# Kernel optimization log

Measured on AMD Instinct MI355X. Metric: run time of the kernel, lower is better.

## Reference

```python
import jax, jax.numpy as jnp
import numpy as np

N, E, F_NODE, F_EDGE = 100000, 400000, 64, 16
HID, HEADS, L, G, FP = 128, 4, 4, 1024, 2048
DH = HID // HEADS
T, K = 5, 32
EPS = 1e-5
NEG_SLOPE = 0.2


def _gat(x, src, dst, ea, Wl, bl, Wr, br, We, att, bias):
    """GATv2Conv (PyG semantics, eval mode): x_l=lin_l(x_src), x_r=lin_r(x_dst),
    e = att . leaky_relu(x_l[src] + x_r[dst] + lin_edge(edge_attr)),
    alpha = segment-softmax over dst, out = scatter-sum(alpha * x_l[src]) + bias."""
    n = x.shape[0]
    xl = (x @ Wl + bl).reshape(n, HEADS, DH)
    xr = (x @ Wr + br).reshape(n, HEADS, DH)
    ee = (ea @ We).reshape(-1, HEADS, DH)
    e = jax.nn.leaky_relu(xl[src] + xr[dst] + ee, NEG_SLOPE)  # [E,H,D]
    score = jnp.einsum('ehd,hd->eh', e, att)                   # [E,H]
    m = jax.ops.segment_max(score, dst, num_segments=n)        # stable softmax
    p = jnp.exp(score - m[dst])
    denom = jax.ops.segment_sum(p, dst, num_segments=n)
    alpha = p / (denom[dst] + 1e-16)
    out = jax.ops.segment_sum(alpha[:, :, None] * xl[src], dst, num_segments=n)
    return out.reshape(n, HID) + bias


def _bn_elu(h, g, b):
    # BatchNorm over the node dimension (training-mode batch stats) + ELU
    mu = h.mean(0)
    var = h.var(0)
    return jax.nn.elu((h - mu) / jnp.sqrt(var + EPS) * g + b)


def setup_inputs() -> dict:
    key = jax.random.key(0)
    ks = jax.random.split(key, 16)
    s_in = 1.0 / np.sqrt(F_NODE)
    s_h = 1.0 / np.sqrt(HID)
    s_e = 1.0 / np.sqrt(F_EDGE)
    Lh = L - 1
    return dict(
        x=jax.random.normal(ks[0], (N, F_NODE), jnp.float32),
        edge_index=jax.random.randint(ks[1], (2, E), 0, N),
        edge_attr=jax.random.normal(ks[2], (E, F_EDGE), jnp.float32),
        batch=jnp.sort(jax.random.randint(ks[3], (N,), 0, G)),
        morgan_fp=(jax.random.uniform(ks[4], (G, FP)) < 0.1).astype(jnp.float32),
        fp_idx=jnp.arange(T * K).reshape(T, K),
        Wl0=jax.random.normal(ks[5], (F_NODE, HID)) * s_in,
        bl0=jnp.zeros((HID,)),
        Wr0=jax.random.normal(ks[6], (F_NODE, HID)) * s_in,
        br0=jnp.zeros((HID,)),
        We0=jax.random.normal(ks[7], (F_EDGE, HID)) * s_e,
        att0=jax.random.normal(ks[8], (HEADS, DH)) * s_h,
        bias0=jnp.zeros((HID,)),
        g0=jnp.ones((HID,)),
        b0=jnp.zeros((HID,)),
        Wl=jax.random.normal(ks[9], (Lh, HID, HID)) * s_h,
        bl=jnp.zeros((Lh, HID)),
        Wr=jax.random.normal(ks[10], (Lh, HID, HID)) * s_h,
        br=jnp.zeros((Lh, HID)),
        We=jax.random.normal(ks[11], (Lh, F_EDGE, HID)) * s_e,
        att=jax.random.normal(ks[12], (Lh, HEADS, DH)) * s_h,
        biasc=jnp.zeros((Lh, HID)),
        g=jnp.ones((Lh, HID)),
        b=jnp.zeros((Lh, HID)),
        tw1=jax.random.normal(ks[13], (T, HID + K, HID)) / np.sqrt(HID + K),
        tb1=jnp.zeros((T, HID)),
        tw2=jax.random.normal(ks[14], (T, HID, 1)) * s_h,
        tb2=jnp.zeros((T, 1)),
    )


def reference(x, edge_index, edge_attr, batch, morgan_fp, fp_idx,
              Wl0, bl0, Wr0, br0, We0, att0, bias0, g0, b0,
              Wl, bl, Wr, br, We, att, biasc, g, b,
              tw1, tb1, tw2, tb2):
    src, dst = edge_index[0], edge_index[1]
    h = _bn_elu(_gat(x, src, dst, edge_attr, Wl0, bl0, Wr0, br0, We0, att0, bias0), g0, b0)
    for i in range(L - 1):  # residual stacked GATv2 layers
        h = _bn_elu(_gat(h, src, dst, edge_attr, Wl[i], bl[i], Wr[i], br[i],
                         We[i], att[i], biasc[i]), g[i], b[i]) + h
    counts = jax.ops.segment_sum(jnp.ones((h.shape[0],), h.dtype), batch, num_segments=G)
    emb = jax.ops.segment_sum(h, batch, num_segments=G) / jnp.maximum(counts, 1.0)[:, None]
    outs = []
    for t in range(T):  # per-task heads on [graph_emb ; selected fp bits]
        fused = jnp.concatenate([emb, morgan_fp[:, fp_idx[t]]], axis=1)
        hm = jax.nn.relu(fused @ tw1[t] + tb1[t])
        outs.append(hm @ tw2[t] + tb2[t])
    return jnp.concatenate(outs, axis=1)  # [G, T]
```

## Files before the change

### kernel.cpp

```cpp
#include <hip/hip_runtime.h>
#include <hip/hip_bf16.h>

#define N_NODES 100000
#define N_EDGES 400000
#define F_NODE_ 64
#define F_EDGE_ 16
#define HID_ 128
#define N_GRAPH 1024
#define N_TASK 5
#define NSTRIPE 32

typedef unsigned short u16;
typedef __attribute__((ext_vector_type(8))) short frag8;
typedef __attribute__((ext_vector_type(4))) float f32x4;
typedef __attribute__((ext_vector_type(2))) float f32x2;

__device__ __forceinline__ float bu2f(u16 v){ return __uint_as_float(((unsigned)v) << 16); }
__device__ __forceinline__ float2 bp2f(unsigned u){
  return make_float2(__uint_as_float(u << 16), __uint_as_float(u & 0xFFFF0000u));
}
__device__ __forceinline__ f32x2 bp2v(unsigned u){
  f32x2 r; r.x = __uint_as_float(u << 16); r.y = __uint_as_float(u & 0xFFFF0000u); return r;
}
__device__ __forceinline__ u16 f2bu(float f){
  __hip_bfloat16 h = __float2bfloat16(f);
  return *(u16*)&h;
}
__device__ __forceinline__ unsigned packbf(float a, float b){
  return (unsigned)f2bu(a) | ((unsigned)f2bu(b) << 16);
}
__device__ __forceinline__ f32x2 pmax2(f32x2 a, f32x2 b){
#if defined(__has_builtin)
#if __has_builtin(__builtin_elementwise_max)
  return __builtin_elementwise_max(a, b);
#else
  f32x2 r; r.x = fmaxf(a.x,b.x); r.y = fmaxf(a.y,b.y); return r;
#endif
#else
  f32x2 r; r.x = fmaxf(a.x,b.x); r.y = fmaxf(a.y,b.y); return r;
#endif
}

struct WZ12 { const float* src[12]; u16* dst[12]; int Ks[12]; int Kd[12]; };

#define CAST_BLKS ((N_NODES*F_NODE_ + 255)/256)
#define EG256 ((N_EDGES + 255)/256)
#define GOFF_BLKS ((N_GRAPH + 1 + 255)/256)
#define WSWZ_BLKS (12*64)
__global__ __launch_bounds__(256) void k_cast_hist(const float* __restrict__ s, u16* __restrict__ d,
                                                   const int* __restrict__ ei, int* __restrict__ counts,
                                                   const int* __restrict__ batch, int* __restrict__ goff,
                                                   WZ12 p){
  int b = blockIdx.x;
  if (b < CAST_BLKS){
    int i = b*256 + threadIdx.x;
    if (i < N_NODES*F_NODE_) d[i] = f2bu(s[i]);
  } else if (b < CAST_BLKS + EG256){
    int e = (b - CAST_BLKS)*256 + threadIdx.x;
    if (e < N_EDGES) atomicAdd(&counts[ei[N_EDGES + e]], 1);
  } else if (b < CAST_BLKS + EG256 + GOFF_BLKS){
    int g = (b - CAST_BLKS - EG256)*256 + threadIdx.x;
    if (g <= N_GRAPH){
      int lo = 0, hi = N_NODES;
      while (lo < hi){
        int mid = (lo + hi) >> 1;
        if (batch[mid] < g) lo = mid + 1; else hi = mid;
      }
      goff[g] = lo;
    }
  } else {
    int bb = b - CAST_BLKS - EG256 - GOFF_BLKS;
    const int sW = bb >> 6;
    const int Kd = p.Kd[sW], Ks = p.Ks[sW];
    int i = (bb & 63)*256 + threadIdx.x;
    if (i >= Kd*128) return;
    int k = i >> 7, n = i & 127;
    float v = (k < Ks) ? p.src[sW][k*128 + n] : 0.f;
    int kk = k & 31, c = k >> 5;
    int quad = kk >> 3, j = kk & 7;
    int nt = n >> 4;
    int lane = quad*16 + (n & 15);
    p.dst[sW][(((c*8 + nt)*64) + lane)*8 + j] = f2bu(v);
  }
}

#define GEMM_GRID ((N_NODES + 127)/128)
#define EPROJ_GRID ((N_EDGES + 127)/128)
__global__ __launch_bounds__(256) void k_gemm_eproj(const u16* __restrict__ A,
                                                    const u16* __restrict__ Wzl,
                                                    const u16* __restrict__ Wzr,
                                                    const float* __restrict__ bl,
                                                    const float* __restrict__ br,
                                                    u16* __restrict__ Cl,
                                                    u16* Cr,
                                                    int M, int K,
                                                    const u16* __restrict__ ea16,
                                                    const u16* __restrict__ Wez,
                                                    u16* __restrict__ eproj){
  __shared__ u16 WS[128*128];
  const int t = threadIdx.x;
  const int b = blockIdx.x;
  if (b < 2*GEMM_GRID){
    const int which = (b >= GEMM_GRID);
    const int bx = which ? b - GEMM_GRID : b;
    const u16*   Wz   = which ? Wzr : Wzl;
    const float* bias = which ? br  : bl;
    u16*         C    = which ? Cr  : Cl;
    {
      const uint4* src = (const uint4*)Wz;
      uint4* dst = (uint4*)WS;
      const int n = (K*128) >> 3;
      for (int i = t; i < n; i += 256) dst[i] = src[i];
    }
    __syncthreads();
    const int w = t >> 6, l = t & 63;
    const int m = l & 15, quad = l >> 4;
    const int rowA0 = bx*128 + w*32 + m;
    const int rowA1 = rowA0 + 16;
    f32x4 acc[2][8];
    #pragma unroll
    for (int i=0;i<2;i++)
      #pragma unroll
      for (int j=0;j<8;j++) acc[i][j] = (f32x4){0.f,0.f,0.f,0.f};
    const int KC = K >> 5;
    for (int c = 0; c < KC; c++){
      frag8 a0 = {}, a1 = {};
      if (rowA0 < M) a0 = *(const frag8*)(A + (size_t)rowA0*K + c*32 + quad*8);
      if (rowA1 < M) a1 = *(const frag8*)(A + (size_t)rowA1*K + c*32 + quad*8);
      #pragma unroll
      for (int nt = 0; nt < 8; nt++){
        frag8 bfr = *(const frag8*)&WS[(((c*8 + nt)*64) + l)*8];
        acc[0][nt] = __builtin_amdgcn_mfma_f32_16x16x32_bf16(a0, bfr, acc[0][nt], 0,0,0);
        acc[1][nt] = __builtin_amdgcn_mfma_f32_16x16x32_bf16(a1, bfr, acc[1][nt], 0,0,0);
      }
    }
    float bcv[8];
    #pragma unroll
    for (int nt=0; nt<8; nt++) bcv[nt] = bias[nt*16 + m];
    __syncthreads();
    const int sXor = quad << 4;
    #pragma unroll
    for (int rt = 0; rt < 2; rt++){
      #pragma unroll
      for (int r = 0; r < 4; r++){
        const int row = w*32 + rt*16 + quad*4 + r;
        #pragma unroll
        for (int nt = 0; nt < 8; nt++){
          const int col = nt*16 + m;
          WS[row*128 + (col ^ sXor)] = f2bu(acc[rt][nt][r] + bcv[nt]);
        }
      }
    }
    __syncthreads();
    #pragma unroll
    for (int i = 0; i < 8; i++){
      const int idx = i*256 + t;
      const int row = idx >> 4, k16 = idx & 15;
      const int grp = (k16*8) ^ (((row>>2)&3)<<4);
      const int grow = bx*128 + row;
      if (grow < M)
        *(uint4*)(C + (size_t)grow*128 + k16*8) = *(const uint4*)&WS[row*128 + grp];
    }
  } else {
    const int bx = b - 2*GEMM_GRID;
    {
      const uint4* s4 = (const uint4*)Wez;
      uint4* d4 = (uint4*)WS;
      for (int i = t; i < 512; i += 256) d4[i] = s4[i];
    }
    __syncthreads();
    const int w = t >> 6, l = t & 63, m = l & 15, quad = l >> 4;
    const int row0 = bx*128 + w*32 + m;
    const int row1 = row0 + 16;
    f32x4 acc[2][8];
    #pragma unroll
    for (int i=0;i<2;i++)
      #pragma unroll
      for (int j=0;j<8;j++) acc[i][j] = (f32x4){0.f,0.f,0.f,0.f};
    frag8 a0 = {}, a1 = {};
    if (quad < 2){
      a0 = *(const frag8*)(ea16 + (size_t)row0*16 + quad*8);
      a1 = *(const frag8*)(ea16 + (size_t)row1*16 + quad*8);
    }
    #pragma unroll
    for (int nt = 0; nt < 8; nt++){
      frag8 bfr = *(const frag8*)&WS[(nt*64 + l)*8];
      acc[0][nt] = __builtin_amdgcn_mfma_f32_16x16x32_bf16(a0, bfr, acc[0][nt], 0,0,0);
      acc[1][nt] = __builtin_amdgcn_mfma_f32_16x16x32_bf16(a1, bfr, acc[1][nt], 0,0,0);
    }
    __syncthreads();
    const int sXor = quad << 4;
    #pragma unroll
    for (int rt = 0; rt < 2; rt++){
      #pragma unroll
      for (int r = 0; r < 4; r++){
        const int row = w*32 + rt*16 + quad*4 + r;
        #pragma unroll
        for (int nt = 0; nt < 8; nt++){
          const int col = nt*16 + m;
          WS[row*128 + (col ^ sXor)] = f2bu(acc[rt][nt][r]);
        }
      }
    }
    __syncthreads();
    #pragma unroll
    for (int i = 0; i < 8; i++){
      const int idx = i*256 + t;
      const int row = idx >> 4, k16 = idx & 15;
      const int grp = (k16*8) ^ (((row>>2)&3)<<4);
      *(uint4*)(eproj + ((size_t)(bx*128 + row))*128 + k16*8) = *(const uint4*)&WS[row*128 + grp];
    }
  }
}

__global__ __launch_bounds__(512) void k_scan1(const int* __restrict__ counts,
                                               int* __restrict__ incl,
                                               int* __restrict__ bsum){
  __shared__ int s[512];
  const int t = threadIdx.x;
  int i = blockIdx.x*512 + t;
  int v = (i < N_NODES) ? counts[i] : 0;
  s[t] = v;
  __syncthreads();
  for (int off = 1; off < 512; off <<= 1){
    int x = (t >= off) ? s[t - off] : 0;
    __syncthreads();
    s[t] += x;
    __syncthreads();
  }
  if (i < N_NODES) incl[i] = s[t];
  if (t == 511) bsum[blockIdx.x] = s[511];
}

__global__ __launch_bounds__(512) void k_scan3(const int* __restrict__ counts,
                                               const int* __restrict__ incl,
                                               const int* __restrict__ bsum, int nb,
                                               int* __restrict__ offsets,
                                               int* __restrict__ cursor){
  __shared__ int sb[256];
  const int t = threadIdx.x;
  if (t < 256) sb[t] = (t < nb) ? bsum[t] : 0;
  __syncthreads();
  for (int off = 1; off < 256; off <<= 1){
    int x = 0;
    if (t < 256 && t >= off) x = sb[t - off];
    __syncthreads();
    if (t < 256) sb[t] += x;
    __syncthreads();
  }
  int i = blockIdx.x*512 + t;
  if (i >= N_NODES) return;
  int pre = (blockIdx.x == 0) ? 0 : sb[blockIdx.x - 1];
  int o = pre + incl[i];
  offsets[i + 1] = o;
  cursor[i]      = o - counts[i];
  if (i == 0) offsets[0] = 0;
}

__global__ __launch_bounds__(256) void k_scatter(const int* __restrict__ ei,
                                                 int* __restrict__ cursor,
                                                 int* __restrict__ ssrc,
                                                 const float* __restrict__ ea,
                                                 u16* __restrict__ ea16){
  int e = blockIdx.x*256 + threadIdx.x;
  if (e >= N_EDGES) return;
  int dst = ei[N_EDGES + e];
  int pos = atomicAdd(&cursor[dst], 1);
  ssrc[pos] = ei[e];
  const float* s = ea + (size_t)e*F_EDGE_;
  unsigned p[8];
  #pragma unroll
  for (int k=0;k<8;k++) p[k] = packbf(s[2*k], s[2*k+1]);
  uint4* d4 = (uint4*)(ea16 + (size_t)pos*16);
  d4[0] = make_uint4(p[0],p[1],p[2],p[3]);
  d4[1] = make_uint4(p[4],p[5],p[6],p[7]);
}

#define GAT_GRID (N_NODES/8)
__global__ __launch_bounds__(128) void k_gat_ep(const u16* __restrict__ xl,
                                                unsigned* xr_aggr,
                                                const u16* __restrict__ eproj,
                                                const float* __restrict__ att,
                                                const int* __restrict__ offsets,
                                                const int* __restrict__ ssrc,
                                                float* __restrict__ stats){
  __shared__ float red[4][264];
  const int t = threadIdx.x;
  const int wave = t >> 6, lane = t & 63;
  const int half = lane >> 5, l32 = lane & 31;
  const int c0 = l32*4;
  const float4 av = *(const float4*)(att + c0);
  const f32x2 avlo = {av.x, av.y}, avhi = {av.z, av.w};
  float ss0=0.f, ss1=0.f, ss2=0.f, ss3=0.f;
  float qq0=0.f, qq1=0.f, qq2=0.f, qq3=0.f;

  for (int k = 0; k < 2; k++){
    const int node = blockIdx.x*8 + wave*4 + k*2 + half;
    const uint2 xru = *(const uint2*)(xr_aggr + (size_t)node*64 + l32*2);
    const f32x2 xr0 = bp2v(xru.x), xr1 = bp2v(xru.y);
    f32x2 acc0 = {0.f,0.f}, acc1 = {0.f,0.f};
    float den = 0.f;
    const int beg = offsets[node], end = offsets[node+1];
    int it = (end - beg + 3) >> 2;
    int oit = __shfl_xor(it, 32);
    const int maxit = it > oit ? it : oit;
    int i = beg;
    for (int n = 0; n < maxit; n++, i += 4){
      const int mm = end - i;
      int ib = (mm > 0) ? i : beg;
      ib = ib < N_EDGES ? ib : N_EDGES - 1;
      const int i0 = ib;
      const int i1 = (mm > 1) ? i+1 : ib;
      const int i2 = (mm > 2) ? i+2 : ib;
      const int i3 = (mm > 3) ? i+3 : ib;
      const int s0 = ssrc[i0], s1 = ssrc[i1], s2 = ssrc[i2], s3 = ssrc[i3];
      const uint2 e0 = *(const uint2*)(eproj + (size_t)i0*128 + c0);
      const uint2 e1 = *(const uint2*)(eproj + (size_t)i1*128 + c0);
      const uint2 e2 = *(const uint2*)(eproj + (size_t)i2*128 + c0);
      const uint2 e3 = *(const uint2*)(eproj + (size_t)i3*128 + c0);
      const uint2 x0 = *(const uint2*)(xl + (size_t)s0*HID_ + c0);
      const uint2 x1 = *(const uint2*)(xl + (size_t)s1*HID_ + c0);
      const uint2 x2 = *(const uint2*)(xl + (size_t)s2*HID_ + c0);
      const uint2 x3 = *(const uint2*)(xl + (size_t)s3*HID_ + c0);
      const f32x2 vl00 = bp2v(x0.x), vl01 = bp2v(x0.y);
      const f32x2 vl10 = bp2v(x1.x), vl11 = bp2v(x1.y);
      const f32x2 vl20 = bp2v(x2.x), vl21 = bp2v(x2.y);
      const f32x2 vl30 = bp2v(x3.x), vl31 = bp2v(x3.y);
      f32x2 v00 = vl00 + xr0 + bp2v(e0.x), v01 = vl01 + xr1 + bp2v(e0.y);
      f32x2 v10 = vl10 + xr0 + bp2v(e1.x), v11 = vl11 + xr1 + bp2v(e1.y);
      f32x2 v20 = vl20 + xr0 + bp2v(e2.x), v21 = vl21 + xr1 + bp2v(e2.y);
      f32x2 v30 = vl30 + xr0 + bp2v(e3.x), v31 = vl31 + xr1 + bp2v(e3.y);
      v00 = pmax2(v00, v00*0.2f); v01 = pmax2(v01, v01*0.2f);
      v10 = pmax2(v10, v10*0.2f); v11 = pmax2(v11, v11*0.2f);
      v20 = pmax2(v20, v20*0.2f); v21 = pmax2(v21, v21*0.2f);
      v30 = pmax2(v30, v30*0.2f); v31 = pmax2(v31, v31*0.2f);
      f32x2 ps0 = v00*avlo + v01*avhi;
      f32x2 ps1 = v10*avlo + v11*avhi;
      f32x2 ps2 = v20*avlo + v21*avhi;
      f32x2 ps3 = v30*avlo + v31*avhi;
      float sc0 = ps0.x + ps0.y;
      float sc1 = ps1.x + ps1.y;
      float sc2 = ps2.x + ps2.y;
      float sc3 = ps3.x + ps3.y;
      sc0 += __shfl_xor(sc0, 1); sc1 += __shfl_xor(sc1, 1); sc2 += __shfl_xor(sc2, 1); sc3 += __shfl_xor(sc3, 1);
      sc0 += __shfl_xor(sc0, 2); sc1 += __shfl_xor(sc1, 2); sc2 += __shfl_xor(sc2, 2); sc3 += __shfl_xor(sc3, 2);
      sc0 += __shfl_xor(sc0, 4); sc1 += __shfl_xor(sc1, 4); sc2 += __shfl_xor(sc2, 4); sc3 += __shfl_xor(sc3, 4);
      const float p0 = (mm > 0) ? __expf(sc0) : 0.f;
      const float p1 = (mm > 1) ? __expf(sc1) : 0.f;
      const float p2 = (mm > 2) ? __expf(sc2) : 0.f;
      const float p3 = (mm > 3) ? __expf(sc3) : 0.f;
      acc0 += p0*vl00 + p1*vl10 + p2*vl20 + p3*vl30;
      acc1 += p0*vl01 + p1*vl11 + p2*vl21 + p3*vl31;
      den  += p0 + p1 + p2 + p3;
    }
    const float inv = 1.0f / (den + 1e-16f);
    uint2 outv;
    outv.x = packbf(acc0.x*inv, acc0.y*inv);
    outv.y = packbf(acc1.x*inv, acc1.y*inv);
    *(uint2*)(xr_aggr + (size_t)node*64 + l32*2) = outv;
    const float2 o0 = bp2f(outv.x), o1 = bp2f(outv.y);
    ss0 += o0.x; ss1 += o0.y; ss2 += o1.x; ss3 += o1.y;
    qq0 += o0.x*o0.x; qq1 += o0.y*o0.y; qq2 += o1.x*o1.x; qq3 += o1.y*o1.y;
  }
  const int g = wave*2 + half;
  red[g][c0+0] = ss0; red[g][c0+1] = ss1; red[g][c0+2] = ss2; red[g][c0+3] = ss3;
  red[g][128+c0+0] = qq0; red[g][128+c0+1] = qq1; red[g][128+c0+2] = qq2; red[g][128+c0+3] = qq3;
  __syncthreads();
  {
    float a = 0.f, b2 = 0.f;
    #pragma unroll
    for (int gg = 0; gg < 4; gg++){ a += red[gg][t]; b2 += red[gg][128+t]; }
    const int base = (blockIdx.x & (NSTRIPE-1))*256;
    atomicAdd(&stats[base + t],       a);
    atomicAdd(&stats[base + 128 + t], b2);
  }
}

__global__ __launch_bounds__(256) void k_bn_apply(const unsigned* __restrict__ aggr_b,
                                                  const float* __restrict__ stats,
                                                  const float* __restrict__ gamma,
                                                  const float* __restrict__ beta,
                                                  u16* __restrict__ h, int residual){
  __shared__ float sc_sh[128], sh_sh[128];
  const int t = threadIdx.x;
  if (t < 128){
    float s = 0.f, q = 0.f;
    #pragma unroll
    for (int st = 0; st < NSTRIPE; st++){
      s += stats[st*256 + t];
      q += stats[st*256 + 128 + t];
    }
    const float invn = 1.0f / (float)N_NODES;
    float mu = s * invn;
    float var = q * invn - mu*mu;
    float sc = rsqrtf(var + 1e-5f) * gamma[t];
    sc_sh[t] = sc;
    sh_sh[t] = beta[t] - mu * sc;
  }
  __syncthreads();
  size_t i = (size_t)blockIdx.x*256 + t;
  if (i >= (size_t)N_NODES*16) return;
  const int c = (int)((i & 15) * 8);
  uint4 v4 = ((const uint4*)aggr_b)[i];
  uint4* hp = (uint4*)h + i;
  uint4 hv4 = make_uint4(0,0,0,0);
  if (residual) hv4 = *hp;
  unsigned vin[4]  = {v4.x, v4.y, v4.z, v4.w};
  unsigned hin[4]  = {hv4.x, hv4.y, hv4.z, hv4.w};
  unsigned outw[4];
  #pragma unroll
  for (int j=0;j<4;j++){
    int cc = c + j*2;
    float2 v = bp2f(vin[j]);
    float val0 = v.x * sc_sh[cc]   + sh_sh[cc];
    float val1 = v.y * sc_sh[cc+1] + sh_sh[cc+1];
    val0 = val0 > 0.f ? val0 : expm1f(val0);
    val1 = val1 > 0.f ? val1 : expm1f(val1);
    if (residual){
      float2 hv = bp2f(hin[j]);
      val0 += hv.x; val1 += hv.y;
    }
    outw[j] = packbf(val0, val1);
  }
  *hp = make_uint4(outw[0], outw[1], outw[2], outw[3]);
}

__global__ __launch_bounds__(256) void k_pool_seg(const unsigned* __restrict__ h2,
                                                  const int* __restrict__ goff,
                                                  float* __restrict__ emb){
  __shared__ float redS[4][128];
  const int g = blockIdx.x, t = threadIdx.x;
  const int p = t & 63, rg = t >> 6;
  const int beg = goff[g], end = goff[g+1];
  float a0 = 0.f, a1 = 0.f;
  for (int r = beg + rg; r < end; r += 4){
    float2 v = bp2f(h2[(size_t)r*64 + p]);
    a0 += v.x; a1 += v.y;
  }
  redS[rg][p*2] = a0; redS[rg][p*2+1] = a1;
  __syncthreads();
  if (rg == 0){
    #pragma unroll
    for (int k=1;k<4;k++){ a0 += redS[k][p*2]; a1 += redS[k][p*2+1]; }
    float n = fmaxf((float)(end - beg), 1.f);
    emb[(size_t)g*HID_ + p*2]     = a0 / n;
    emb[(size_t)g*HID_ + p*2 + 1] = a1 / n;
  }
}

#define HG 8
__global__ __launch_bounds__(128) void k_heads(const float* __restrict__ emb,
                                               const float* __restrict__ mf,
                                               const int* __restrict__ fpi,
                                               const float* __restrict__ tw1,
                                               const float* __restrict__ tb1,
                                               const float* __restrict__ tw2,
                                               const float* __restrict__ tb2,
                                               float* __restrict__ out){
  const int task = blockIdx.y, g0 = blockIdx.x*HG;
  const int j = threadIdx.x;
  __shared__ float fused[HG][160];
  __shared__ float red[HG][128];
  for (int idx = j; idx < HG*160; idx += 128){
    int g = idx / 160, i = idx % 160;
    float v;
    if (i < 128) v = emb[(size_t)(g0+g)*HID_ + i];
    else         v = mf[(size_t)(g0+g)*2048 + fpi[task*32 + (i-128)]];
    fused[g][i] = v;
  }
  __syncthreads();
  const float* w1 = tw1 + (size_t)task*160*128;
  float acc[HG];
  float b1 = tb1[task*128 + j];
  #pragma unroll
  for (int g=0; g<HG; g++) acc[g] = b1;
  for (int i=0; i<160; i++){
    float wv = w1[(size_t)i*128 + j];
    #pragma unroll
    for (int g=0; g<HG; g++) acc[g] += fused[g][i] * wv;
  }
  float t2 = tw2[task*128 + j];
  #pragma unroll
  for (int g=0; g<HG; g++){
    float v = acc[g] > 0.f ? acc[g] : 0.f;
    red[g][j] = v * t2;
  }
  __syncthreads();
  int g = j >> 4, l16 = j & 15;
  float s = 0.f;
  #pragma unroll
  for (int k=0;k<8;k++) s += red[g][l16 + k*16];
  s += __shfl_xor(s, 1, 16);
  s += __shfl_xor(s, 2, 16);
  s += __shfl_xor(s, 4, 16);
  s += __shfl_xor(s, 8, 16);
  if (l16 == 0) out[(size_t)(g0+g)*N_TASK + task] = s + tb2[task];
}

extern "C" void kernel_launch(void* const* d_in, const int* in_sizes, int n_in,
                              void* d_out, int out_size, void* d_ws, size_t ws_size,
                              hipStream_t stream){
  const float* x    = (const float*)d_in[0];
  const int*   ei   = (const int*)  d_in[1];
  const float* ea   = (const float*)d_in[2];
  const int*   batch= (const int*)  d_in[3];
  const float* mf   = (const float*)d_in[4];
  const int*   fpi  = (const int*)  d_in[5];
  const float* Wl0  = (const float*)d_in[6];
  const float* bl0  = (const float*)d_in[7];
  const float* Wr0  = (const float*)d_in[8];
  const float* br0  = (const float*)d_in[9];
  const float* We0  = (const float*)d_in[10];
  const float* att0 = (const float*)d_in[11];
  const float* g0   = (const float*)d_in[13];
  const float* b0   = (const float*)d_in[14];
  const float* Wl   = (const float*)d_in[15];
  const float* bl   = (const float*)d_in[16];
  const float* Wr   = (const float*)d_in[17];
  const float* br   = (const float*)d_in[18];
  const float* We   = (const float*)d_in[19];
  const float* att  = (const float*)d_in[20];
  const float* gg   = (const float*)d_in[22];
  const float* bb   = (const float*)d_in[23];
  const float* tw1  = (const float*)d_in[24];
  const float* tb1  = (const float*)d_in[25];
  const float* tw2  = (const float*)d_in[26];
  const float* tb2  = (const float*)d_in[27];
  float* out = (float*)d_out;

  char* w = (char*)d_ws;
  auto alloc = [&](size_t bytes)->char*{ char* r = w; w += (bytes + 255) & ~(size_t)255; return r; };
  u16*   xl     = (u16*)  alloc((size_t)N_NODES*HID_*2);
  unsigned* xr_aggr = (unsigned*)alloc((size_t)N_NODES*64*4);
  u16*   h      = (u16*)  alloc((size_t)N_NODES*HID_*2);
  u16*   ea16   = (u16*)  alloc((size_t)N_EDGES*16*2);
  int*   counts = (int*)  alloc((size_t)N_NODES*4);
  float* stats4 = (float*)alloc(4*NSTRIPE*256*4);
  int*   offsets= (int*)  alloc((size_t)(N_NODES+1)*4);
  int*   cursor = (int*)  alloc((size_t)N_NODES*4);
  int*   incl   = (int*)  alloc((size_t)N_NODES*4);
  int*   bsum   = (int*)  alloc(256*4);
  int*   ssrc   = (int*)  alloc((size_t)N_EDGES*4);
  int*   goff   = (int*)  alloc((size_t)(N_GRAPH+1)*4);
  float* emb    = (float*)alloc((size_t)N_GRAPH*HID_*4);
  u16*   Wzl0   = (u16*)  alloc((size_t)F_NODE_*128*2);
  u16*   Wzr0   = (u16*)  alloc((size_t)F_NODE_*128*2);
  u16*   Wzl123 = (u16*)  alloc((size_t)3*HID_*128*2);
  u16*   Wzr123 = (u16*)  alloc((size_t)3*HID_*128*2);
  u16*   Wez4   = (u16*)  alloc((size_t)4*32*128*2);
  u16*   eproj  = (u16*)  alloc((size_t)N_EDGES*HID_*2);
  u16*   xbf    = (u16*)  alloc((size_t)N_NODES*F_NODE_*2);

  const size_t zlen = (size_t)((char*)(stats4 + 4*NSTRIPE*256) - (char*)counts);
  const int nscan = (N_NODES + 511)/512;

  WZ12 p;
  p.src[0] = Wl0; p.dst[0] = Wzl0; p.Ks[0] = F_NODE_; p.Kd[0] = F_NODE_;
  p.src[1] = Wr0; p.dst[1] = Wzr0; p.Ks[1] = F_NODE_; p.Kd[1] = F_NODE_;
  for (int i=0;i<3;i++){
    p.src[2+i] = Wl + (size_t)i*HID_*HID_; p.dst[2+i] = Wzl123 + (size_t)i*HID_*128; p.Ks[2+i] = HID_; p.Kd[2+i] = HID_;
    p.src[5+i] = Wr + (size_t)i*HID_*HID_; p.dst[5+i] = Wzr123 + (size_t)i*HID_*128; p.Ks[5+i] = HID_; p.Kd[5+i] = HID_;
  }
  p.src[8] = We0; p.dst[8] = Wez4; p.Ks[8] = F_EDGE_; p.Kd[8] = 32;
  for (int i=0;i<3;i++){
    p.src[9+i] = We + (size_t)i*F_EDGE_*HID_; p.dst[9+i] = Wez4 + (size_t)(i+1)*32*128; p.Ks[9+i] = F_EDGE_; p.Kd[9+i] = 32;
  }

  hipMemsetAsync(counts, 0, zlen, stream);
  hipLaunchKernelGGL(k_cast_hist, dim3(CAST_BLKS + EG256 + GOFF_BLKS + WSWZ_BLKS), dim3(256), 0, stream,
                     x, xbf, ei, counts, batch, goff, p);
  hipLaunchKernelGGL(k_scan1,  dim3(nscan), dim3(512), 0, stream, counts, incl, bsum);
  hipLaunchKernelGGL(k_scan3,  dim3(nscan), dim3(512), 0, stream, counts, incl, bsum, nscan, offsets, cursor);
  hipLaunchKernelGGL(k_scatter,dim3(EG256), dim3(256), 0, stream, ei, cursor, ssrc, ea, ea16);

  for (int layer = 0; layer < 4; layer++){
    const float *bl_, *br_, *att_, *g_, *b_;
    const u16 *Wzl_, *Wzr_, *Ain;
    int K;
    if (layer == 0){
      bl_=bl0; br_=br0; att_=att0; g_=g0; b_=b0;
      Wzl_ = Wzl0; Wzr_ = Wzr0; Ain = xbf; K = F_NODE_;
    } else {
      int i = layer - 1;
      bl_ = bl + (size_t)i*HID_;  br_ = br + (size_t)i*HID_;
      att_= att + (size_t)i*HID_;
      g_  = gg + (size_t)i*HID_;  b_  = bb + (size_t)i*HID_;
      Wzl_ = Wzl123 + (size_t)i*HID_*128;
      Wzr_ = Wzr123 + (size_t)i*HID_*128;
      Ain = h; K = HID_;
    }
    float* stats = stats4 + (size_t)layer*NSTRIPE*256;
    hipLaunchKernelGGL(k_gemm_eproj, dim3(2*GEMM_GRID + EPROJ_GRID), dim3(256), 0, stream,
                       Ain, Wzl_, Wzr_, bl_, br_, xl, (u16*)xr_aggr, N_NODES, K,
                       ea16, Wez4 + (size_t)layer*32*128, eproj);
    hipLaunchKernelGGL(k_gat_ep, dim3(GAT_GRID), dim3(128), 0, stream,
                       xl, xr_aggr, eproj, att_, offsets, ssrc, stats);
    hipLaunchKernelGGL(k_bn_apply, dim3((N_NODES*16 + 255)/256), dim3(256), 0, stream,
                       xr_aggr, stats, g_, b_, h, layer > 0 ? 1 : 0);
  }
  hipLaunchKernelGGL(k_pool_seg, dim3(N_GRAPH), dim3(256), 0, stream, (const unsigned*)h, goff, emb);
  hipLaunchKernelGGL(k_heads, dim3(N_GRAPH/HG, N_TASK), dim3(128), 0, stream, emb, mf, fpi, tw1, tb1, tw2, tb2, out);
}
```

Baseline: 641.7 us.

## Process GAT nodes in degree-sorted order to balance per-wave edge loops

Builds a degree histogram during the scan, computes per-degree offsets, and counting-sorts node ids by in-degree into an order array. The GAT edge-processing kernel then maps each half-wave to a node taken from this order. Paired half-waves and waves in a block therefore get similar degrees, which cuts the idle lanes from the max-iteration loop. The cost is an extra indirection per node and scattered memory access to xr/aggr rows instead of sequential ones.

```diff
diff --git a/kernel.cpp b/kernel.cpp
--- a/kernel.cpp
+++ b/kernel.cpp
@@ -45,6 +45,7 @@
 
 #define CAST_BLKS ((N_NODES*F_NODE_ + 255)/256)
 #define EG256 ((N_EDGES + 255)/256)
+#define NG256 ((N_NODES + 255)/256)
 #define GOFF_BLKS ((N_GRAPH + 1 + 255)/256)
 #define WSWZ_BLKS (12*64)
 __global__ __launch_bounds__(256) void k_cast_hist(const float* __restrict__ s, u16* __restrict__ d,
@@ -215,13 +216,20 @@
 
 __global__ __launch_bounds__(512) void k_scan1(const int* __restrict__ counts,
                                                int* __restrict__ incl,
-                                               int* __restrict__ bsum){
+                                               int* __restrict__ bsum,
+                                               int* __restrict__ dhist){
   __shared__ int s[512];
+  __shared__ int lh[256];
   const int t = threadIdx.x;
+  if (t < 256) lh[t] = 0;
   int i = blockIdx.x*512 + t;
   int v = (i < N_NODES) ? counts[i] : 0;
   s[t] = v;
   __syncthreads();
+  if (i < N_NODES){
+    int dgr = v < 255 ? v : 255;
+    atomicAdd(&lh[dgr], 1);
+  }
   for (int off = 1; off < 512; off <<= 1){
     int x = (t >= off) ? s[t - off] : 0;
     __syncthreads();
@@ -230,13 +238,20 @@
   }
   if (i < N_NODES) incl[i] = s[t];
   if (t == 511) bsum[blockIdx.x] = s[511];
+  __syncthreads();
+  if (t < 256){
+    int c = lh[t];
+    if (c) atomicAdd(&dhist[t], c);
+  }
 }
 
 __global__ __launch_bounds__(512) void k_scan3(const int* __restrict__ counts,
                                                const int* __restrict__ incl,
                                                const int* __restrict__ bsum, int nb,
                                                int* __restrict__ offsets,
-                                               int* __restrict__ cursor){
+                                               int* __restrict__ cursor,
+                                               const int* __restrict__ dhist,
+                                               int* __restrict__ dcur){
   __shared__ int sb[256];
   const int t = threadIdx.x;
   if (t < 256) sb[t] = (t < nb) ? bsum[t] : 0;
@@ -249,31 +264,70 @@
     __syncthreads();
   }
   int i = blockIdx.x*512 + t;
-  if (i >= N_NODES) return;
-  int pre = (blockIdx.x == 0) ? 0 : sb[blockIdx.x - 1];
-  int o = pre + incl[i];
-  offsets[i + 1] = o;
-  cursor[i]      = o - counts[i];
-  if (i == 0) offsets[0] = 0;
+  if (i < N_NODES){
+    int pre = (blockIdx.x == 0) ? 0 : sb[blockIdx.x - 1];
+    int o = pre + incl[i];
+    offsets[i + 1] = o;
+    cursor[i]      = o - counts[i];
+    if (i == 0) offsets[0] = 0;
+  }
+  if (blockIdx.x == 0){
+    __syncthreads();
+    int dv = (t < 256) ? dhist[t] : 0;
+    if (t < 256) sb[t] = dv;
+    __syncthreads();
+    for (int off = 1; off < 256; off <<= 1){
+      int x = 0;
+      if (t < 256 && t >= off) x = sb[t - off];
+      __syncthreads();
+      if (t < 256) sb[t] += x;
+      __syncthreads();
+    }
+    if (t < 256) dcur[t] = sb[t] - dv;
+  }
 }
 
 __global__ __launch_bounds__(256) void k_scatter(const int* __restrict__ ei,
                                                  int* __restrict__ cursor,
                                                  int* __restrict__ ssrc,
                                                  const float* __restrict__ ea,
-                                                 u16* __restrict__ ea16){
-  int e = blockIdx.x*256 + threadIdx.x;
-  if (e >= N_EDGES) return;
-  int dst = ei[N_EDGES + e];
-  int pos = atomicAdd(&cursor[dst], 1);
-  ssrc[pos] = ei[e];
-  const float* s = ea + (size_t)e*F_EDGE_;
-  unsigned p[8];
-  #pragma unroll
-  for (int k=0;k<8;k++) p[k] = packbf(s[2*k], s[2*k+1]);
-  uint4* d4 = (uint4*)(ea16 + (size_t)pos*16);
-  d4[0] = make_uint4(p[0],p[1],p[2],p[3]);
-  d4[1] = make_uint4(p[4],p[5],p[6],p[7]);
+                                                 u16* __restrict__ ea16,
+                                                 const int* __restrict__ counts,
+                                                 int* __restrict__ dcur,
+                                                 int* __restrict__ order){
+  __shared__ int lhist[256], gbase[256];
+  const int b = blockIdx.x, t = threadIdx.x;
+  if (b < EG256){
+    int e = b*256 + t;
+    if (e >= N_EDGES) return;
+    int dst = ei[N_EDGES + e];
+    int pos = atomicAdd(&cursor[dst], 1);
+    ssrc[pos] = ei[e];
+    const float* s = ea + (size_t)e*F_EDGE_;
+    unsigned p[8];
+    #pragma unroll
+    for (int k=0;k<8;k++) p[k] = packbf(s[2*k], s[2*k+1]);
+    uint4* d4 = (uint4*)(ea16 + (size_t)pos*16);
+    d4[0] = make_uint4(p[0],p[1],p[2],p[3]);
+    d4[1] = make_uint4(p[4],p[5],p[6],p[7]);
+  } else {
+    const int n = (b - EG256)*256 + t;
+    lhist[t] = 0;
+    __syncthreads();
+    int dgr = 0, lrank = 0;
+    const bool valid = (n < N_NODES);
+    if (valid){
+      dgr = counts[n]; dgr = dgr < 255 ? dgr : 255;
+      lrank = atomicAdd(&lhist[dgr], 1);
+    }
+    __syncthreads();
+    {
+      int c = lhist[t];
+      gbase[t] = (c > 0) ? atomicAdd(&dcur[t], c) : 0;
+    }
+    __syncthreads();
+    if (valid) order[gbase[dgr] + lrank] = n;
+  }
 }
 
 #define GAT_GRID (N_NODES/8)
@@ -283,6 +337,7 @@
                                                 const float* __restrict__ att,
                                                 const int* __restrict__ offsets,
                                                 const int* __restrict__ ssrc,
+                                                const int* __restrict__ order,
                                                 float* __restrict__ stats){
   __shared__ float red[4][264];
   const int t = threadIdx.x;
@@ -295,7 +350,8 @@
   float qq0=0.f, qq1=0.f, qq2=0.f, qq3=0.f;
 
   for (int k = 0; k < 2; k++){
-    const int node = blockIdx.x*8 + wave*4 + k*2 + half;
+    const int gid = blockIdx.x*8 + wave*4 + k*2 + half;
+    const int node = order[gid];
     const uint2 xru = *(const uint2*)(xr_aggr + (size_t)node*64 + l32*2);
     const f32x2 xr0 = bp2v(xru.x), xr1 = bp2v(xru.y);
     f32x2 acc0 = {0.f,0.f}, acc1 = {0.f,0.f};
@@ -536,12 +592,15 @@
   u16*   ea16   = (u16*)  alloc((size_t)N_EDGES*16*2);
   int*   counts = (int*)  alloc((size_t)N_NODES*4);
   float* stats4 = (float*)alloc(4*NSTRIPE*256*4);
+  int*   dhist  = (int*)  alloc(256*4);
   int*   offsets= (int*)  alloc((size_t)(N_NODES+1)*4);
   int*   cursor = (int*)  alloc((size_t)N_NODES*4);
   int*   incl   = (int*)  alloc((size_t)N_NODES*4);
   int*   bsum   = (int*)  alloc(256*4);
   int*   ssrc   = (int*)  alloc((size_t)N_EDGES*4);
   int*   goff   = (int*)  alloc((size_t)(N_GRAPH+1)*4);
+  int*   dcur   = (int*)  alloc(256*4);
+  int*   order  = (int*)  alloc((size_t)N_NODES*4);
   float* emb    = (float*)alloc((size_t)N_GRAPH*HID_*4);
   u16*   Wzl0   = (u16*)  alloc((size_t)F_NODE_*128*2);
   u16*   Wzr0   = (u16*)  alloc((size_t)F_NODE_*128*2);
@@ -551,7 +610,7 @@
   u16*   eproj  = (u16*)  alloc((size_t)N_EDGES*HID_*2);
   u16*   xbf    = (u16*)  alloc((size_t)N_NODES*F_NODE_*2);
 
-  const size_t zlen = (size_t)((char*)(stats4 + 4*NSTRIPE*256) - (char*)counts);
+  const size_t zlen = (size_t)((char*)(dhist + 256) - (char*)counts);
   const int nscan = (N_NODES + 511)/512;
 
   WZ12 p;
@@ -569,9 +628,9 @@
   hipMemsetAsync(counts, 0, zlen, stream);
   hipLaunchKernelGGL(k_cast_hist, dim3(CAST_BLKS + EG256 + GOFF_BLKS + WSWZ_BLKS), dim3(256), 0, stream,
                      x, xbf, ei, counts, batch, goff, p);
-  hipLaunchKernelGGL(k_scan1,  dim3(nscan), dim3(512), 0, stream, counts, incl, bsum);
-  hipLaunchKernelGGL(k_scan3,  dim3(nscan), dim3(512), 0, stream, counts, incl, bsum, nscan, offsets, cursor);
-  hipLaunchKernelGGL(k_scatter,dim3(EG256), dim3(256), 0, stream, ei, cursor, ssrc, ea, ea16);
+  hipLaunchKernelGGL(k_scan1,  dim3(nscan), dim3(512), 0, stream, counts, incl, bsum, dhist);
+  hipLaunchKernelGGL(k_scan3,  dim3(nscan), dim3(512), 0, stream, counts, incl, bsum, nscan, offsets, cursor, dhist, dcur);
+  hipLaunchKernelGGL(k_scatter,dim3(EG256 + NG256), dim3(256), 0, stream, ei, cursor, ssrc, ea, ea16, counts, dcur, order);
 
   for (int layer = 0; layer < 4; layer++){
     const float *bl_, *br_, *att_, *g_, *b_;
@@ -594,7 +653,7 @@
                        Ain, Wzl_, Wzr_, bl_, br_, xl, (u16*)xr_aggr, N_NODES, K,
                        ea16, Wez4 + (size_t)layer*32*128, eproj);
     hipLaunchKernelGGL(k_gat_ep, dim3(GAT_GRID), dim3(128), 0, stream,
-                       xl, xr_aggr, eproj, att_, offsets, ssrc, stats);
+                       xl, xr_aggr, eproj, att_, offsets, ssrc, order, stats);
     hipLaunchKernelGGL(k_bn_apply, dim3((N_NODES*16 + 255)/256), dim3(256), 0, stream,
                        xr_aggr, stats, g_, b_, h, layer > 0 ? 1 : 0);
   }
```

Measured after the change: 649.6 us. Within noise of the previous version (+1.2%).
